# Kernel tuning notes

Measured on AMD Instinct MI355X. Metric: run time of the kernel, lower is better.

The kernel has to match this reference:

```python
import jax, jax.numpy as jnp
import numpy as np

N_HEADS = 16
B = 8
SEQ = 1024
HID = 1024
TOT = B * SEQ


def setup_inputs() -> dict:
    key = jax.random.key(0)
    k1, k2, k3 = jax.random.split(key, 3)
    hidden_states = jax.random.normal(k1, (TOT, HID), dtype=jnp.float32)
    Wqkv = jax.random.normal(k2, (3 * HID, HID), dtype=jnp.float32) * 0.02
    Bqkv = jax.random.normal(k3, (3 * HID,), dtype=jnp.float32) * 0.02
    cu_seqlens = (jnp.arange(B + 1, dtype=jnp.int32) * SEQ)
    return {"hidden_states": hidden_states, "Wqkv": Wqkv, "Bqkv": Bqkv,
            "cu_seqlens": cu_seqlens, "max_s": SEQ}


def reference(hidden_states, Wqkv, Bqkv, cu_seqlens, max_s):
    # qkv projection: F.linear(hidden, Wqkv, Bqkv) -> [T, 3H]
    T, H = hidden_states.shape
    h = N_HEADS
    d = H // h
    b = cu_seqlens.shape[0] - 1
    S = T // b  # equal-length packing; cu_seqlens = arange(b+1)*S
    qkv = hidden_states @ Wqkv.T + Bqkv                      # [T, 3H]
    qkv = qkv.reshape(b, S, 3, h, d)
    q, k, v = qkv[:, :, 0], qkv[:, :, 1], qkv[:, :, 2]       # [b, S, h, d]
    scale = 1.0 / jnp.sqrt(jnp.asarray(d, dtype=q.dtype))
    scores = jnp.einsum("bshd,bthd->bhst", q, k) * scale     # [b, h, S, S]
    probs = jax.nn.softmax(scores, axis=-1)                  # p_dropout = 0.0
    ctx = jnp.einsum("bhst,bthd->bshd", probs, v)            # [b, S, h, d]
    return ctx.reshape(T, H)
```

## Files before the change

kernel.cpp:

```cpp
#include <hip/hip_runtime.h>

typedef __attribute__((ext_vector_type(8))) __bf16 bf16x8;
typedef __attribute__((ext_vector_type(2))) __bf16 bf16x2;
typedef __attribute__((ext_vector_type(4))) float f32x4;
typedef __attribute__((ext_vector_type(4))) unsigned int u32x4;

#define AS1 __attribute__((address_space(1)))
#define AS3 __attribute__((address_space(3)))

__device__ __forceinline__ unsigned short f2b(float f) {
    union { float f; unsigned int u; } c; c.f = f;
    unsigned int r = c.u + 0x7fffu + ((c.u >> 16) & 1u);
    return (unsigned short)(r >> 16);
}

__device__ __forceinline__ unsigned int pack2(float a, float b) {
    bf16x2 t;
    t[0] = (__bf16)a;
    t[1] = (__bf16)b;
    return __builtin_bit_cast(unsigned int, t);
}

__device__ __forceinline__ void gload_lds16(const void* g, void* l) {
    __builtin_amdgcn_global_load_lds((const AS1 unsigned int*)g,
                                     (AS3 unsigned int*)l, 16, 0, 0);
}

__global__ void cvt2_kernel(const float* __restrict__ in0,
                            unsigned short* __restrict__ out0, int n0,
                            const float* __restrict__ in1,
                            unsigned short* __restrict__ out1, int n1) {
    int i = blockIdx.x * blockDim.x + threadIdx.x;
    int stride = gridDim.x * blockDim.x;
    const int nt = n0 + n1;
    for (; i < nt; i += stride) {
        if (i < n0) {
            float4 v = reinterpret_cast<const float4*>(in0)[i];
            ushort4 o;
            o.x = f2b(v.x); o.y = f2b(v.y); o.z = f2b(v.z); o.w = f2b(v.w);
            reinterpret_cast<ushort4*>(out0)[i] = o;
        } else {
            const int j = i - n0;
            float4 v = reinterpret_cast<const float4*>(in1)[j];
            ushort4 o;
            o.x = f2b(v.x); o.y = f2b(v.y); o.z = f2b(v.z); o.w = f2b(v.w);
            reinterpret_cast<ushort4*>(out1)[j] = o;
        }
    }
}

__global__ __launch_bounds__(512, 4) void qkv_gemm(
    const unsigned short* __restrict__ A,
    const unsigned short* __restrict__ Bw,
    const float* __restrict__ bias,
    unsigned short* __restrict__ qb,
    unsigned short* __restrict__ kb,
    unsigned short* __restrict__ vb)
{
    __shared__ __align__(16) char smem[73728];
    const int tid = threadIdx.x;
    const int lane = tid & 63, w = tid >> 6;
    const int wm = w >> 1, wn = w & 1;
    const int wg = (blockIdx.x & 7) * 96 + (blockIdx.x >> 3);
    const int mt = wg / 24;
    const int nt = wg % 24;
    const int fr = lane & 15, kg = lane >> 4;

    const int sr = lane >> 2;
    const int g  = (lane & 3) ^ ((sr >> 1) & 3);
    const unsigned short* a_srcg = A  + (size_t)(mt * 256 + w * 16 + sr) * 1024 + g * 8;
    const unsigned short* b_srcg = Bw + (size_t)(nt * 128 + w * 16 + sr) * 1024 + g * 8;

    f32x4 acc[4][4] = {};
    const int pg = (kg ^ ((fr >> 1) & 3)) * 16;
    const int aoffA = (wm * 64 + fr) * 64;
    const int boffB = (wn * 64 + fr) * 64;

#define STAGE_FULL(buf, kt) do {                                    \
    char* Sb_ = smem + (buf) * 24576 + w * 1024;                    \
    const size_t ko_ = (size_t)(kt) * 32;                           \
    gload_lds16(a_srcg + ko_,          Sb_);                        \
    gload_lds16(a_srcg + 131072 + ko_, Sb_ + 8192);                 \
    gload_lds16(b_srcg + ko_,          Sb_ + 16384);                \
} while (0)

#define MM(m_, n_) do {                                                        \
    acc[m_][n_] = __builtin_amdgcn_mfma_f32_16x16x32_bf16(                     \
        af[m_], bf[n_], acc[m_][n_], 0, 0, 0);                                 \
} while (0)

#define GT2(CUR, PRE, kt, DOSTAGE, WNSTR) do {                                 \
    const char* Ab_ = smem + (CUR) * 24576;                                    \
    const char* Bb_ = Ab_ + 16384;                                             \
    char* Sb_ = smem + (PRE) * 24576 + w * 1024;                               \
    const size_t ko_ = (size_t)((kt) + 2) * 32;                                \
    bf16x8 af[4], bf[4];                                                       \
    _Pragma("unroll")                                                          \
    for (int n = 0; n < 4; ++n)                                                \
        bf[n] = *reinterpret_cast<const bf16x8*>(Bb_ + boffB + n * 1024 + pg); \
    _Pragma("unroll")                                                          \
    for (int m = 0; m < 2; ++m)                                                \
        af[m] = *reinterpret_cast<const bf16x8*>(Ab_ + aoffA + m * 1024 + pg); \
    if (DOSTAGE) {                                                             \
        gload_lds16(a_srcg + ko_,          Sb_);                               \
        gload_lds16(a_srcg + 131072 + ko_, Sb_ + 8192);                        \
    }                                                                          \
    __builtin_amdgcn_s_barrier();                                              \
    asm volatile("s_waitcnt lgkmcnt(0)" ::: "memory");                         \
    __builtin_amdgcn_s_setprio(1);                                             \
    MM(0, 0); MM(0, 1); MM(0, 2); MM(0, 3);                                    \
    MM(1, 0); MM(1, 1); MM(1, 2); MM(1, 3);                                    \
    __builtin_amdgcn_s_setprio(0);                                             \
    _Pragma("unroll")                                                          \
    for (int m = 2; m < 4; ++m)                                                \
        af[m] = *reinterpret_cast<const bf16x8*>(Ab_ + aoffA + m * 1024 + pg); \
    if (DOSTAGE) {                                                             \
        gload_lds16(b_srcg + ko_, Sb_ + 16384);                                \
    }                                                                          \
    asm volatile("s_waitcnt vmcnt(" WNSTR ") lgkmcnt(0)" ::: "memory");        \
    __builtin_amdgcn_s_barrier();                                              \
    __builtin_amdgcn_s_setprio(1);                                             \
    MM(2, 0); MM(2, 1); MM(2, 2); MM(2, 3);                                    \
    MM(3, 0); MM(3, 1); MM(3, 2); MM(3, 3);                                    \
    __builtin_amdgcn_s_setprio(0);                                             \
} while (0)

    STAGE_FULL(0, 0);
    STAGE_FULL(1, 1);
    asm volatile("s_waitcnt vmcnt(3)" ::: "memory");
    __builtin_amdgcn_s_barrier();
#pragma unroll 1
    for (int it = 0; it < 10; ++it) {
        const int t0 = it * 3;
        GT2(0, 2, t0 + 0, 1, "3");
        GT2(1, 0, t0 + 1, 1, "3");
        GT2(2, 1, t0 + 2, 1, "3");
    }
    GT2(0, 2, 30, 0, "0");
    GT2(1, 0, 31, 0, "0");
    __syncthreads();

    const int sidx = nt >> 3;
    float bv[4];
#pragma unroll
    for (int n = 0; n < 4; ++n) bv[n] = bias[nt * 128 + wn * 64 + n * 16 + fr];

    unsigned short* Cs = (unsigned short*)smem;

    if (sidx < 2) {
        unsigned short* dstb = (sidx == 0) ? qb : kb;
        const float sc = (sidx == 0) ? 0.1803368801111f : 1.0f;
#pragma unroll
        for (int p = 0; p < 2; ++p) {
            if ((wm >> 1) == p) {
                const int r0 = (wm & 1) * 64;
#pragma unroll
                for (int m = 0; m < 4; ++m)
#pragma unroll
                    for (int n = 0; n < 4; ++n)
#pragma unroll
                        for (int r = 0; r < 4; ++r)
                            Cs[(r0 + m * 16 + kg * 4 + r) * 136 + wn * 64 + n * 16 + fr] =
                                f2b((acc[m][n][r] + bv[n]) * sc);
            }
            __syncthreads();
#pragma unroll
            for (int itc = 0; itc < 4; ++itc) {
                const int task = itc * 512 + tid;
                const int rl = task >> 4;
                const int i16 = task & 15;
                const int t = mt * 256 + p * 128 + rl;
                const int b_ = t >> 10, s = t & 1023;
                const int head = ((nt * 128 + i16 * 8) >> 6) & 15;
                u32x4 v = *reinterpret_cast<const u32x4*>(Cs + rl * 136 + i16 * 8);
                *reinterpret_cast<u32x4*>(
                    dstb + ((size_t)(b_ * 16 + head) * 1024 + s) * 64 + (i16 & 7) * 8) = v;
            }
            __syncthreads();
        }
    } else {
#pragma unroll
        for (int p = 0; p < 2; ++p) {
            if ((wm >> 1) == p) {
                const int r0 = (wm & 1) * 64;
#pragma unroll
                for (int m = 0; m < 4; ++m)
#pragma unroll
                    for (int n = 0; n < 4; ++n)
#pragma unroll
                        for (int j = 0; j < 2; ++j) {
                            unsigned int pk = pack2(acc[m][n][2 * j] + bv[n],
                                                    acc[m][n][2 * j + 1] + bv[n]);
                            *reinterpret_cast<unsigned int*>(
                                Cs + (wn * 64 + n * 16 + fr) * 136
                                   + r0 + m * 16 + kg * 4 + 2 * j) = pk;
                        }
            }
            __syncthreads();
#pragma unroll
            for (int itc = 0; itc < 4; ++itc) {
                const int task = itc * 512 + tid;
                const int c = task >> 4;
                const int i16 = task & 15;
                const int col = nt * 128 + c;
                const int head = (col >> 6) & 15;
                const int d = col & 63;
                const int b_ = (mt * 256) >> 10;
                const int s0 = (mt * 256 & 1023) + p * 128 + i16 * 8;
                u32x4 v = *reinterpret_cast<const u32x4*>(Cs + c * 136 + i16 * 8);
                *reinterpret_cast<u32x4*>(
                    vb + (size_t)((b_ * 16 + head) * 64 + d) * 1024 + s0) = v;
            }
            __syncthreads();
        }
    }
#undef STAGE_FULL
#undef GT2
#undef MM
}

#define KVB 64
__global__ __launch_bounds__(256, 4) void attn_kernel(
    const unsigned short* __restrict__ qb,
    const unsigned short* __restrict__ kb,
    const unsigned short* __restrict__ vb,
    float* __restrict__ out)
{
    __shared__ __align__(16) char asmem[32768];
    const int tid = threadIdx.x;
    const int lane = tid & 63, w = tid >> 6;
    const int wg = (blockIdx.x & 7) * 128 + (blockIdx.x >> 3);
    const int bh = wg >> 3;
    const int qt = wg & 7;
    const int b_ = bh >> 4, h_ = bh & 15;
    const int fr = lane & 15, kg = lane >> 4;

    const unsigned short* qp = qb + ((size_t)bh * 1024 + qt * 128) * 64;
    const unsigned short* kp = kb + (size_t)bh * 1024 * 64;
    const unsigned short* vp = vb + (size_t)bh * 64 * 1024;

    bf16x8 qfr[2][2];
#pragma unroll
    for (int qf = 0; qf < 2; ++qf) {
        const unsigned short* qr = qp + (w * 32 + qf * 16 + fr) * 64 + kg * 8;
        qfr[qf][0] = *reinterpret_cast<const bf16x8*>(qr);
        qfr[qf][1] = *reinterpret_cast<const bf16x8*>(qr + 32);
    }

    float m_q[2] = {-1e30f, -1e30f}, l_q[2] = {0.f, 0.f};
    f32x4 o_acc[2][4] = {};

    const int ksr = w * 8 + (lane >> 3);
    const int kcb = (lane & 7) * 16;

#define ASTAGE(buf, kvt) do {                                                  \
    const int kv0_ = (kvt) * KVB;                                              \
    char* Kb_ = asmem + (buf) * 16384 + w * 1024;                              \
    char* Vb_ = Kb_ + 8192;                                                    \
    _Pragma("unroll")                                                          \
    for (int i = 0; i < 2; ++i) {                                              \
        const int st = i * 32 + ksr;                                           \
        const int key = ((st >> 5) << 5) | (((st & 15) >> 2) << 3)             \
                      | (((st >> 4) & 1) << 2) | (st & 3);                     \
        const int scb = kcb ^ ((st & 7) << 4);                                 \
        gload_lds16(kp + (size_t)(kv0_ + key) * 64 + (scb >> 1),               \
                    Kb_ + i * 4096);                                           \
        const int d_ = i * 32 + ksr;                                           \
        const int svb = kcb ^ ((d_ & 7) << 4);                                 \
        gload_lds16(vp + (size_t)d_ * 1024 + kv0_ + (svb >> 1),                \
                    Vb_ + i * 4096);                                           \
    }                                                                          \
} while (0)

#define ACOMP(buf) do {                                                        \
    const char* Kb = asmem + (buf) * 16384;                                    \
    const char* Vb = Kb + 8192;                                                \
    f32x4 sacc[2][4] = {};                                                     \
    __builtin_amdgcn_s_setprio(1);                                             \
    _Pragma("unroll")                                                          \
    for (int jt = 0; jt < 4; ++jt) {                                           \
        _Pragma("unroll")                                                      \
        for (int ks = 0; ks < 2; ++ks) {                                       \
            const int cb = (ks * 64 + kg * 16) ^ ((fr & 7) << 4);              \
            bf16x8 kf = *reinterpret_cast<const bf16x8*>(                      \
                Kb + (jt * 16 + fr) * 128 + cb);                               \
            _Pragma("unroll")                                                  \
            for (int qf = 0; qf < 2; ++qf)                                     \
                sacc[qf][jt] = __builtin_amdgcn_mfma_f32_16x16x32_bf16(        \
                    kf, qfr[qf][ks], sacc[qf][jt], 0, 0, 0);                   \
        }                                                                      \
    }                                                                          \
    __builtin_amdgcn_s_setprio(0);                                             \
    unsigned int P2[2][4][2];                                                  \
    _Pragma("unroll")                                                          \
    for (int qf = 0; qf < 2; ++qf) {                                           \
        float mx = -1e30f;                                                     \
        _Pragma("unroll")                                                      \
        for (int jt = 0; jt < 4; ++jt) {                                       \
            float a = fmaxf(fmaxf(sacc[qf][jt][0], sacc[qf][jt][1]),           \
                            fmaxf(sacc[qf][jt][2], sacc[qf][jt][3]));          \
            mx = fmaxf(mx, a);                                                 \
        }                                                                      \
        mx = fmaxf(mx, __shfl_xor(mx, 16, 64));                                \
        mx = fmaxf(mx, __shfl_xor(mx, 32, 64));                                \
        if (__any(mx > m_q[qf] + 8.0f)) {                                      \
            const float mn = fmaxf(m_q[qf], mx);                               \
            const float corr = __builtin_amdgcn_exp2f(m_q[qf] - mn);           \
            m_q[qf] = mn;                                                      \
            l_q[qf] *= corr;                                                   \
            float cr[4];                                                       \
            _Pragma("unroll")                                                  \
            for (int r = 0; r < 4; ++r)                                        \
                cr[r] = __shfl(corr, kg * 4 + r, 64);                          \
            _Pragma("unroll")                                                  \
            for (int d0 = 0; d0 < 4; ++d0)                                     \
                _Pragma("unroll")                                              \
                for (int r = 0; r < 4; ++r) o_acc[qf][d0][r] *= cr[r];         \
        }                                                                      \
        const float mn_ = m_q[qf];                                             \
        float rs = 0.f;                                                        \
        _Pragma("unroll")                                                      \
        for (int jt = 0; jt < 4; ++jt) {                                       \
            float p0 = __builtin_amdgcn_exp2f(sacc[qf][jt][0] - mn_);          \
            float p1 = __builtin_amdgcn_exp2f(sacc[qf][jt][1] - mn_);          \
            float p2 = __builtin_amdgcn_exp2f(sacc[qf][jt][2] - mn_);          \
            float p3 = __builtin_amdgcn_exp2f(sacc[qf][jt][3] - mn_);          \
            rs += (p0 + p1) + (p2 + p3);                                       \
            P2[qf][jt][0] = pack2(p0, p1);                                     \
            P2[qf][jt][1] = pack2(p2, p3);                                     \
        }                                                                      \
        rs += __shfl_xor(rs, 16, 64);                                          \
        rs += __shfl_xor(rs, 32, 64);                                          \
        l_q[qf] += rs;                                                         \
    }                                                                          \
    __builtin_amdgcn_s_setprio(1);                                             \
    _Pragma("unroll")                                                          \
    for (int c = 0; c < 2; ++c) {                                              \
        bf16x8 pa[2];                                                          \
        _Pragma("unroll")                                                      \
        for (int qf = 0; qf < 2; ++qf) {                                       \
            u32x4 pw = { P2[qf][2 * c][0], P2[qf][2 * c][1],                   \
                         P2[qf][2 * c + 1][0], P2[qf][2 * c + 1][1] };         \
            pa[qf] = __builtin_bit_cast(bf16x8, pw);                           \
        }                                                                      \
        _Pragma("unroll")                                                      \
        for (int d0 = 0; d0 < 4; ++d0) {                                       \
            const int dd = d0 * 16 + fr;                                       \
            const int cbv = (c * 64 + kg * 16) ^ ((dd & 7) << 4);              \
            bf16x8 vf = *reinterpret_cast<const bf16x8*>(Vb + dd * 128 + cbv); \
            _Pragma("unroll")                                                  \
            for (int qf = 0; qf < 2; ++qf)                                     \
                o_acc[qf][d0] = __builtin_amdgcn_mfma_f32_16x16x32_bf16(       \
                    pa[qf], vf, o_acc[qf][d0], 0, 0, 0);                       \
        }                                                                      \
    }                                                                          \
    __builtin_amdgcn_s_setprio(0);                                             \
} while (0)

    ASTAGE(0, 0);
#pragma unroll 1
    for (int t = 0; t < 15; ++t) {
        ASTAGE((t + 1) & 1, t + 1);
        asm volatile("s_waitcnt vmcnt(4) lgkmcnt(0)" ::: "memory");
        __builtin_amdgcn_s_barrier();
        ACOMP(t & 1);
        asm volatile("s_waitcnt lgkmcnt(0)" ::: "memory");
        __builtin_amdgcn_s_barrier();
    }
    asm volatile("s_waitcnt vmcnt(0) lgkmcnt(0)" ::: "memory");
    __builtin_amdgcn_s_barrier();
    ACOMP(1);

#pragma unroll
    for (int qf = 0; qf < 2; ++qf) {
        float linv[4];
#pragma unroll
        for (int r = 0; r < 4; ++r)
            linv[r] = 1.0f / __shfl(l_q[qf], kg * 4 + r, 64);
        const int trow = b_ * 1024 + qt * 128 + w * 32 + qf * 16;
#pragma unroll
        for (int d0 = 0; d0 < 4; ++d0) {
            const int c = h_ * 64 + d0 * 16 + fr;
#pragma unroll
            for (int r = 0; r < 4; ++r)
                out[(size_t)(trow + kg * 4 + r) * 1024 + c] = o_acc[qf][d0][r] * linv[r];
        }
    }
#undef ASTAGE
#undef ACOMP
}

extern "C" void kernel_launch(void* const* d_in, const int* in_sizes, int n_in,
                              void* d_out, int out_size, void* d_ws, size_t ws_size,
                              hipStream_t stream)
{
    const float* hs   = (const float*)d_in[0];
    const float* Wqkv = (const float*)d_in[1];
    const float* Bqkv = (const float*)d_in[2];
    float* out = (float*)d_out;

    char* ws = (char*)d_ws;
    unsigned short* hsb = (unsigned short*)(ws);
    unsigned short* wb  = (unsigned short*)(ws + (size_t)16 * 1048576);
    unsigned short* qb  = (unsigned short*)(ws + (size_t)22 * 1048576);
    unsigned short* kb  = (unsigned short*)(ws + (size_t)38 * 1048576);
    unsigned short* vb  = (unsigned short*)(ws + (size_t)54 * 1048576);

    cvt2_kernel<<<2048, 256, 0, stream>>>(hs, hsb, 8192 * 1024 / 4,
                                          Wqkv, wb, 3072 * 1024 / 4);
    qkv_gemm<<<768, 512, 0, stream>>>(hsb, wb, Bqkv, qb, kb, vb);
    attn_kernel<<<1024, 256, 0, stream>>>(qb, kb, vb, out);
}
```

Measured before the change: 120.2 us.

## Read K/V fragments directly from global memory in attention, dropping LDS staging

The attention kernel no longer stages K and V tiles through double-buffered shared memory with async global-to-LDS loads and barriers. Each wave now loads its MFMA K and V fragments straight from global memory (through the caches), which removes the LDS round trip and the per-iteration barriers. In exchange, each of the four waves reloads the same K/V data, so global and cache traffic rises, and there is no explicit prefetch to hide load latency behind compute.

```diff
diff --git a/kernel.cpp b/kernel.cpp
--- a/kernel.cpp
+++ b/kernel.cpp
@@ -226,7 +226,6 @@
     const unsigned short* __restrict__ vb,
     float* __restrict__ out)
 {
-    __shared__ __align__(16) char asmem[32768];
     const int tid = threadIdx.x;
     const int lane = tid & 63, w = tid >> 6;
     const int wg = (blockIdx.x & 7) * 128 + (blockIdx.x >> 3);
@@ -250,40 +249,21 @@
     float m_q[2] = {-1e30f, -1e30f}, l_q[2] = {0.f, 0.f};
     f32x4 o_acc[2][4] = {};
 
-    const int ksr = w * 8 + (lane >> 3);
-    const int kcb = (lane & 7) * 16;
-
-#define ASTAGE(buf, kvt) do {                                                  \
+    const int rbase = (fr >> 2) * 8 + (fr & 3);
+    const unsigned short* kfp = kp + (size_t)rbase * 64 + kg * 8;
+    const unsigned short* vfp = vp + (size_t)fr * 1024 + kg * 8;
+
+#define ACOMPG(kvt) do {                                                       \
     const int kv0_ = (kvt) * KVB;                                              \
-    char* Kb_ = asmem + (buf) * 16384 + w * 1024;                              \
-    char* Vb_ = Kb_ + 8192;                                                    \
-    _Pragma("unroll")                                                          \
-    for (int i = 0; i < 2; ++i) {                                              \
-        const int st = i * 32 + ksr;                                           \
-        const int key = ((st >> 5) << 5) | (((st & 15) >> 2) << 3)             \
-                      | (((st >> 4) & 1) << 2) | (st & 3);                     \
-        const int scb = kcb ^ ((st & 7) << 4);                                 \
-        gload_lds16(kp + (size_t)(kv0_ + key) * 64 + (scb >> 1),               \
-                    Kb_ + i * 4096);                                           \
-        const int d_ = i * 32 + ksr;                                           \
-        const int svb = kcb ^ ((d_ & 7) << 4);                                 \
-        gload_lds16(vp + (size_t)d_ * 1024 + kv0_ + (svb >> 1),                \
-                    Vb_ + i * 4096);                                           \
-    }                                                                          \
-} while (0)
-
-#define ACOMP(buf) do {                                                        \
-    const char* Kb = asmem + (buf) * 16384;                                    \
-    const char* Vb = Kb + 8192;                                                \
     f32x4 sacc[2][4] = {};                                                     \
     __builtin_amdgcn_s_setprio(1);                                             \
     _Pragma("unroll")                                                          \
     for (int jt = 0; jt < 4; ++jt) {                                           \
+        const int jo = (jt >> 1) * 32 + (jt & 1) * 4;                          \
         _Pragma("unroll")                                                      \
         for (int ks = 0; ks < 2; ++ks) {                                       \
-            const int cb = (ks * 64 + kg * 16) ^ ((fr & 7) << 4);              \
             bf16x8 kf = *reinterpret_cast<const bf16x8*>(                      \
-                Kb + (jt * 16 + fr) * 128 + cb);                               \
+                kfp + (size_t)(kv0_ + jo) * 64 + ks * 32);                     \
             _Pragma("unroll")                                                  \
             for (int qf = 0; qf < 2; ++qf)                                     \
                 sacc[qf][jt] = __builtin_amdgcn_mfma_f32_16x16x32_bf16(        \
@@ -345,9 +325,8 @@
         }                                                                      \
         _Pragma("unroll")                                                      \
         for (int d0 = 0; d0 < 4; ++d0) {                                       \
-            const int dd = d0 * 16 + fr;                                       \
-            const int cbv = (c * 64 + kg * 16) ^ ((dd & 7) << 4);              \
-            bf16x8 vf = *reinterpret_cast<const bf16x8*>(Vb + dd * 128 + cbv); \
+            bf16x8 vf = *reinterpret_cast<const bf16x8*>(                      \
+                vfp + (size_t)(d0 * 16) * 1024 + kv0_ + c * 32);               \
             _Pragma("unroll")                                                  \
             for (int qf = 0; qf < 2; ++qf)                                     \
                 o_acc[qf][d0] = __builtin_amdgcn_mfma_f32_16x16x32_bf16(       \
@@ -357,19 +336,10 @@
     __builtin_amdgcn_s_setprio(0);                                             \
 } while (0)
 
-    ASTAGE(0, 0);
 #pragma unroll 1
-    for (int t = 0; t < 15; ++t) {
-        ASTAGE((t + 1) & 1, t + 1);
-        asm volatile("s_waitcnt vmcnt(4) lgkmcnt(0)" ::: "memory");
-        __builtin_amdgcn_s_barrier();
-        ACOMP(t & 1);
-        asm volatile("s_waitcnt lgkmcnt(0)" ::: "memory");
-        __builtin_amdgcn_s_barrier();
-    }
-    asm volatile("s_waitcnt vmcnt(0) lgkmcnt(0)" ::: "memory");
-    __builtin_amdgcn_s_barrier();
-    ACOMP(1);
+    for (int t = 0; t < 16; ++t) {
+        ACOMPG(t);
+    }
 
 #pragma unroll
     for (int qf = 0; qf < 2; ++qf) {
@@ -386,8 +356,7 @@
                 out[(size_t)(trow + kg * 4 + r) * 1024 + c] = o_acc[qf][d0][r] * linv[r];
         }
     }
-#undef ASTAGE
-#undef ACOMP
+#undef ACOMPG
 }
 
 extern "C" void kernel_launch(void* const* d_in, const int* in_sizes, int n_in,
```

After: 187.8 us. 56.2% more time.

## Software-pipeline attention loop: overlap next-tile QK^T with current softmax and PV

Applied to the files above, without the earlier changes.

Splits the combined K/V staging and compute into separate K and V stages plus separate QK^T and softmax·V phases. The main loop is restructured so that the QK^T MFMAs for tile t+1 are issued alongside the softmax and PV work for tile t, using ping-pong score registers. K is prefetched two tiles ahead and V one tile ahead, with one barrier per iteration instead of two. The aim is to overlap MFMA work with exp and shuffle work and cut synchronization, at the cost of extra registers for a second score buffer and a fully drained vmcnt(0) wait each iteration.

```diff
diff --git a/kernel.cpp b/kernel.cpp
--- a/kernel.cpp
+++ b/kernel.cpp
@@ -253,10 +253,9 @@
     const int ksr = w * 8 + (lane >> 3);
     const int kcb = (lane & 7) * 16;
 
-#define ASTAGE(buf, kvt) do {                                                  \
+#define KSTAGE(bufi, kvt) do {                                                 \
     const int kv0_ = (kvt) * KVB;                                              \
-    char* Kb_ = asmem + (buf) * 16384 + w * 1024;                              \
-    char* Vb_ = Kb_ + 8192;                                                    \
+    char* Kb_ = asmem + (bufi) * 8192 + w * 1024;                              \
     _Pragma("unroll")                                                          \
     for (int i = 0; i < 2; ++i) {                                              \
         const int st = i * 32 + ksr;                                           \
@@ -265,6 +264,14 @@
         const int scb = kcb ^ ((st & 7) << 4);                                 \
         gload_lds16(kp + (size_t)(kv0_ + key) * 64 + (scb >> 1),               \
                     Kb_ + i * 4096);                                           \
+    }                                                                          \
+} while (0)
+
+#define VSTAGE(bufi, kvt) do {                                                 \
+    const int kv0_ = (kvt) * KVB;                                              \
+    char* Vb_ = asmem + 16384 + (bufi) * 8192 + w * 1024;                      \
+    _Pragma("unroll")                                                          \
+    for (int i = 0; i < 2; ++i) {                                              \
         const int d_ = i * 32 + ksr;                                           \
         const int svb = kcb ^ ((d_ & 7) << 4);                                 \
         gload_lds16(vp + (size_t)d_ * 1024 + kv0_ + (svb >> 1),                \
@@ -272,10 +279,12 @@
     }                                                                          \
 } while (0)
 
-#define ACOMP(buf) do {                                                        \
-    const char* Kb = asmem + (buf) * 16384;                                    \
-    const char* Vb = Kb + 8192;                                                \
-    f32x4 sacc[2][4] = {};                                                     \
+#define AQKT(bufi, S) do {                                                     \
+    const char* Kb = asmem + (bufi) * 8192;                                    \
+    _Pragma("unroll")                                                          \
+    for (int qf = 0; qf < 2; ++qf)                                             \
+        _Pragma("unroll")                                                      \
+        for (int jt = 0; jt < 4; ++jt) { f32x4 z_ = {}; S[qf][jt] = z_; }      \
     __builtin_amdgcn_s_setprio(1);                                             \
     _Pragma("unroll")                                                          \
     for (int jt = 0; jt < 4; ++jt) {                                           \
@@ -286,19 +295,23 @@
                 Kb + (jt * 16 + fr) * 128 + cb);                               \
             _Pragma("unroll")                                                  \
             for (int qf = 0; qf < 2; ++qf)                                     \
-                sacc[qf][jt] = __builtin_amdgcn_mfma_f32_16x16x32_bf16(        \
-                    kf, qfr[qf][ks], sacc[qf][jt], 0, 0, 0);                   \
+                S[qf][jt] = __builtin_amdgcn_mfma_f32_16x16x32_bf16(           \
+                    kf, qfr[qf][ks], S[qf][jt], 0, 0, 0);                      \
         }                                                                      \
     }                                                                          \
     __builtin_amdgcn_s_setprio(0);                                             \
+} while (0)
+
+#define ASMPV(bufi, S) do {                                                    \
+    const char* Vb = asmem + 16384 + (bufi) * 8192;                            \
     unsigned int P2[2][4][2];                                                  \
     _Pragma("unroll")                                                          \
     for (int qf = 0; qf < 2; ++qf) {                                           \
         float mx = -1e30f;                                                     \
         _Pragma("unroll")                                                      \
         for (int jt = 0; jt < 4; ++jt) {                                       \
-            float a = fmaxf(fmaxf(sacc[qf][jt][0], sacc[qf][jt][1]),           \
-                            fmaxf(sacc[qf][jt][2], sacc[qf][jt][3]));          \
+            float a = fmaxf(fmaxf(S[qf][jt][0], S[qf][jt][1]),                 \
+                            fmaxf(S[qf][jt][2], S[qf][jt][3]));                \
             mx = fmaxf(mx, a);                                                 \
         }                                                                      \
         mx = fmaxf(mx, __shfl_xor(mx, 16, 64));                                \
@@ -321,10 +334,10 @@
         float rs = 0.f;                                                        \
         _Pragma("unroll")                                                      \
         for (int jt = 0; jt < 4; ++jt) {                                       \
-            float p0 = __builtin_amdgcn_exp2f(sacc[qf][jt][0] - mn_);          \
-            float p1 = __builtin_amdgcn_exp2f(sacc[qf][jt][1] - mn_);          \
-            float p2 = __builtin_amdgcn_exp2f(sacc[qf][jt][2] - mn_);          \
-            float p3 = __builtin_amdgcn_exp2f(sacc[qf][jt][3] - mn_);          \
+            float p0 = __builtin_amdgcn_exp2f(S[qf][jt][0] - mn_);             \
+            float p1 = __builtin_amdgcn_exp2f(S[qf][jt][1] - mn_);             \
+            float p2 = __builtin_amdgcn_exp2f(S[qf][jt][2] - mn_);             \
+            float p3 = __builtin_amdgcn_exp2f(S[qf][jt][3] - mn_);             \
             rs += (p0 + p1) + (p2 + p3);                                       \
             P2[qf][jt][0] = pack2(p0, p1);                                     \
             P2[qf][jt][1] = pack2(p2, p3);                                     \
@@ -357,19 +370,33 @@
     __builtin_amdgcn_s_setprio(0);                                             \
 } while (0)
 
-    ASTAGE(0, 0);
+#define ITER(kt, KRB, VRB, KWB, VWB, SC, SN, DOKST) do {                       \
+    asm volatile("s_waitcnt vmcnt(0) lgkmcnt(0)" ::: "memory");                \
+    __builtin_amdgcn_s_barrier();                                              \
+    if (DOKST) KSTAGE(KWB, (kt) + 2);                                          \
+    VSTAGE(VWB, (kt) + 1);                                                     \
+    AQKT(KRB, SN);                                                             \
+    ASMPV(VRB, SC);                                                            \
+} while (0)
+
+    KSTAGE(0, 0);
+    VSTAGE(0, 0);
+    KSTAGE(1, 1);
+    asm volatile("s_waitcnt vmcnt(2)" ::: "memory");
+    __builtin_amdgcn_s_barrier();
+    f32x4 sA[2][4], sB[2][4];
+    AQKT(0, sA);
+
 #pragma unroll 1
-    for (int t = 0; t < 15; ++t) {
-        ASTAGE((t + 1) & 1, t + 1);
-        asm volatile("s_waitcnt vmcnt(4) lgkmcnt(0)" ::: "memory");
-        __builtin_amdgcn_s_barrier();
-        ACOMP(t & 1);
-        asm volatile("s_waitcnt lgkmcnt(0)" ::: "memory");
-        __builtin_amdgcn_s_barrier();
-    }
+    for (int it = 0; it < 7; ++it) {
+        const int t0 = 2 * it;
+        ITER(t0,     1, 0, 0, 1, sA, sB, 1);
+        ITER(t0 + 1, 0, 1, 1, 0, sB, sA, 1);
+    }
+    ITER(14, 1, 0, 0, 1, sA, sB, 0);
     asm volatile("s_waitcnt vmcnt(0) lgkmcnt(0)" ::: "memory");
     __builtin_amdgcn_s_barrier();
-    ACOMP(1);
+    ASMPV(1, sB);
 
 #pragma unroll
     for (int qf = 0; qf < 2; ++qf) {
@@ -386,8 +413,11 @@
                 out[(size_t)(trow + kg * 4 + r) * 1024 + c] = o_acc[qf][d0][r] * linv[r];
         }
     }
-#undef ASTAGE
-#undef ACOMP
+#undef KSTAGE
+#undef VSTAGE
+#undef AQKT
+#undef ASMPV
+#undef ITER
 }
 
 extern "C" void kernel_launch(void* const* d_in, const int* in_sizes, int n_in,
```

Measured after the change: 215.9 us. 79.6% more time.
